# Optimization experiments

Hardware: AMD Instinct MI355X
Metric: run time of the kernel (lower is better)

## Reference

```python
import jax, jax.numpy as jnp
import numpy as np

B, V, H, K = 2048, 4096, 1024, 5

def setup_inputs() -> dict:
    key = jax.random.key(0)
    k1, k2, k3, k4, k5, k6, k7 = jax.random.split(key, 7)
    return {
        "visible_example": (jax.random.uniform(k1, (B, V)) > 0.5).astype(jnp.float32),
        "b_v": jax.random.normal(k2, (V,), jnp.float32) * 0.1,
        "b_h": jax.random.normal(k3, (H,), jnp.float32) * 0.1,
        "W": jax.random.normal(k4, (V, H), jnp.float32) * 0.02,
        "u_h0": jax.random.uniform(k5, (B, H), jnp.float32),
        "u_v": jax.random.uniform(k6, (K // 2 + 1, B, V), jnp.float32),
        "u_h": jax.random.uniform(k7, (K // 2, B, H), jnp.float32),
    }

def reference(visible_example, b_v, b_h, W, u_h0, u_v, u_h):
    # score(v,h) = -energy = v.b_v + h.b_h + (v @ W) * h summed
    def score(v, h):
        return v @ b_v + h @ b_h + jnp.einsum('bv,vh,bh->b', v, W, h)  # [B]

    def bernoulli(p, u):
        # samples are detached in the original (requires_grad_(False))
        return jax.lax.stop_gradient((p > u).astype(jnp.float32))

    # positive phase: sample h | data
    h = bernoulli(jax.nn.sigmoid(b_h + visible_example @ W), u_h0)  # [B,H]
    log_prob_positive = score(visible_example, h)

    # K-step alternating Gibbs chain: v, h, v, h, v  (statically unrolled)
    v = visible_example
    vi = hi = 0
    for k in range(K):
        if k % 2 == 0:
            v = bernoulli(jax.nn.sigmoid(b_v + h @ W.T), u_v[vi]); vi += 1
        else:
            h = bernoulli(jax.nn.sigmoid(b_h + v @ W), u_h[hi]); hi += 1

    log_prob_negative = score(v, h)
    return log_prob_positive - log_prob_negative  # [B]
```

## Files before the change

kernel.cpp:

```cpp
#include <hip/hip_runtime.h>
#include <math.h>

#define B_DIM 2048
#define V_DIM 4096
#define H_DIM 1024

#define BM 64
#define BN 64
#define BK 16
#define KC 384
#define LDS_STRIDE 68

enum { ACC_NONE = 0, ACC_PREACT = 1, ACC_BIAS = 2 };

__global__ __launch_bounds__(256) void gemm_h_kernel(
    const float* __restrict__ A,
    const float* __restrict__ W,
    const float* __restrict__ bh,
    const float* __restrict__ U,
    float* __restrict__ Hout,
    double* __restrict__ acc,
    const int mode)
{
    __shared__ float As[2][BK][LDS_STRIDE];
    __shared__ float Bs[2][BK][LDS_STRIDE];

    const int bn = blockIdx.x * BN;
    const int bm = blockIdx.y * BM;
    const int t  = threadIdx.x;
    const int tx = t & 15;
    const int ty = t >> 4;

    const int ar  = t >> 2;
    const int ac4 = t & 3;
    const int br  = t >> 4;
    const int bc4 = t & 15;

    float tot[4][4];
    float part[4][4];
#pragma unroll
    for (int i = 0; i < 4; i++)
#pragma unroll
        for (int j = 0; j < 4; j++) { tot[i][j] = 0.0f; part[i][j] = 0.0f; }

    const float* Aptr = A + (size_t)(bm + ar) * V_DIM + ac4 * 4;
    const float* Wptr = W + (size_t)bn + bc4 * 4;

    float4 av = *(const float4*)(Aptr + 0);
    float4 wv = *(const float4*)(Wptr + (size_t)br * H_DIM);
    As[0][ac4 * 4 + 0][ar] = av.x;
    As[0][ac4 * 4 + 1][ar] = av.y;
    As[0][ac4 * 4 + 2][ar] = av.z;
    As[0][ac4 * 4 + 3][ar] = av.w;
    *(float4*)(&Bs[0][br][bc4 * 4]) = wv;

    const int T = V_DIM / BK;
    int cur = 0;
    for (int it = 0; it < T; ++it) {
        __syncthreads();
        if (it + 1 < T) {
            const int k0 = (it + 1) * BK;
            av = *(const float4*)(Aptr + k0);
            wv = *(const float4*)(Wptr + (size_t)(k0 + br) * H_DIM);
        }
#pragma unroll
        for (int k = 0; k < BK; k++) {
            float4 a4 = *(const float4*)(&As[cur][k][ty * 4]);
            float4 b4 = *(const float4*)(&Bs[cur][k][tx * 4]);
            float aa[4] = {a4.x, a4.y, a4.z, a4.w};
            float bb[4] = {b4.x, b4.y, b4.z, b4.w};
#pragma unroll
            for (int i = 0; i < 4; i++)
#pragma unroll
                for (int j = 0; j < 4; j++)
                    part[i][j] = fmaf(aa[i], bb[j], part[i][j]);
        }
        if (it + 1 < T) {
            As[cur ^ 1][ac4 * 4 + 0][ar] = av.x;
            As[cur ^ 1][ac4 * 4 + 1][ar] = av.y;
            As[cur ^ 1][ac4 * 4 + 2][ar] = av.z;
            As[cur ^ 1][ac4 * 4 + 3][ar] = av.w;
            *(float4*)(&Bs[cur ^ 1][br][bc4 * 4]) = wv;
        }
        cur ^= 1;
        if ((((it + 1) * BK) % KC) == 0) {
#pragma unroll
            for (int i = 0; i < 4; i++)
#pragma unroll
                for (int j = 0; j < 4; j++) { tot[i][j] += part[i][j]; part[i][j] = 0.0f; }
        }
    }
    if ((V_DIM % KC) != 0) {
#pragma unroll
        for (int i = 0; i < 4; i++)
#pragma unroll
            for (int j = 0; j < 4; j++) tot[i][j] += part[i][j];
    }

    double rowacc[4] = {0.0, 0.0, 0.0, 0.0};
#pragma unroll
    for (int i = 0; i < 4; i++) {
        const int row = bm + ty * 4 + i;
#pragma unroll
        for (int j = 0; j < 4; j++) {
            const int col = bn + tx * 4 + j;
            float bias = bh[col];
            float pre = bias + tot[i][j];
            float p = 1.0f / (1.0f + expf(-pre));
            float u = U[(size_t)row * H_DIM + col];
            float hv = (p > u) ? 1.0f : 0.0f;
            Hout[(size_t)row * H_DIM + col] = hv;
            if (mode == ACC_PREACT) rowacc[i] += (double)hv * (double)pre;
            else if (mode == ACC_BIAS) rowacc[i] += (double)hv * (double)bias;
        }
    }
    if (mode != ACC_NONE) {
#pragma unroll
        for (int off = 8; off >= 1; off >>= 1)
#pragma unroll
            for (int i = 0; i < 4; i++)
                rowacc[i] += __shfl_xor(rowacc[i], off, 16);
        if (tx == 0) {
#pragma unroll
            for (int i = 0; i < 4; i++)
                atomicAdd(&acc[bm + ty * 4 + i], rowacc[i]);
        }
    }
}

__global__ __launch_bounds__(256) void gemm_v_kernel(
    const float* __restrict__ A,
    const float* __restrict__ W,
    const float* __restrict__ bv,
    const float* __restrict__ U,
    float* __restrict__ Vout,
    double* __restrict__ acc,
    const int mode)
{
    __shared__ float As[2][BK][LDS_STRIDE];
    __shared__ float Bs[2][BK][LDS_STRIDE];

    const int bn = blockIdx.x * BN;
    const int bm = blockIdx.y * BM;
    const int t  = threadIdx.x;
    const int tx = t & 15;
    const int ty = t >> 4;

    const int ar  = t >> 2;
    const int ac4 = t & 3;

    float tot[4][4];
    float part[4][4];
#pragma unroll
    for (int i = 0; i < 4; i++)
#pragma unroll
        for (int j = 0; j < 4; j++) { tot[i][j] = 0.0f; part[i][j] = 0.0f; }

    const float* Aptr = A + (size_t)(bm + ar) * H_DIM + ac4 * 4;
    const float* Wrow = W + (size_t)(bn + ar) * H_DIM + ac4 * 4;

    float4 av = *(const float4*)(Aptr + 0);
    float4 wv = *(const float4*)(Wrow + 0);
    As[0][ac4 * 4 + 0][ar] = av.x;
    As[0][ac4 * 4 + 1][ar] = av.y;
    As[0][ac4 * 4 + 2][ar] = av.z;
    As[0][ac4 * 4 + 3][ar] = av.w;
    Bs[0][ac4 * 4 + 0][ar] = wv.x;
    Bs[0][ac4 * 4 + 1][ar] = wv.y;
    Bs[0][ac4 * 4 + 2][ar] = wv.z;
    Bs[0][ac4 * 4 + 3][ar] = wv.w;

    const int T = H_DIM / BK;
    int cur = 0;
    for (int it = 0; it < T; ++it) {
        __syncthreads();
        if (it + 1 < T) {
            const int k0 = (it + 1) * BK;
            av = *(const float4*)(Aptr + k0);
            wv = *(const float4*)(Wrow + k0);
        }
#pragma unroll
        for (int k = 0; k < BK; k++) {
            float4 a4 = *(const float4*)(&As[cur][k][ty * 4]);
            float4 b4 = *(const float4*)(&Bs[cur][k][tx * 4]);
            float aa[4] = {a4.x, a4.y, a4.z, a4.w};
            float bb[4] = {b4.x, b4.y, b4.z, b4.w};
#pragma unroll
            for (int i = 0; i < 4; i++)
#pragma unroll
                for (int j = 0; j < 4; j++)
                    part[i][j] = fmaf(aa[i], bb[j], part[i][j]);
        }
        if (it + 1 < T) {
            As[cur ^ 1][ac4 * 4 + 0][ar] = av.x;
            As[cur ^ 1][ac4 * 4 + 1][ar] = av.y;
            As[cur ^ 1][ac4 * 4 + 2][ar] = av.z;
            As[cur ^ 1][ac4 * 4 + 3][ar] = av.w;
            Bs[cur ^ 1][ac4 * 4 + 0][ar] = wv.x;
            Bs[cur ^ 1][ac4 * 4 + 1][ar] = wv.y;
            Bs[cur ^ 1][ac4 * 4 + 2][ar] = wv.z;
            Bs[cur ^ 1][ac4 * 4 + 3][ar] = wv.w;
        }
        cur ^= 1;
        if ((((it + 1) * BK) % KC) == 0) {
#pragma unroll
            for (int i = 0; i < 4; i++)
#pragma unroll
                for (int j = 0; j < 4; j++) { tot[i][j] += part[i][j]; part[i][j] = 0.0f; }
        }
    }
    if ((H_DIM % KC) != 0) {
#pragma unroll
        for (int i = 0; i < 4; i++)
#pragma unroll
            for (int j = 0; j < 4; j++) tot[i][j] += part[i][j];
    }

    double rowacc[4] = {0.0, 0.0, 0.0, 0.0};
#pragma unroll
    for (int i = 0; i < 4; i++) {
        const int row = bm + ty * 4 + i;
#pragma unroll
        for (int j = 0; j < 4; j++) {
            const int col = bn + tx * 4 + j;
            float pre = bv[col] + tot[i][j];
            float p = 1.0f / (1.0f + expf(-pre));
            float u = U[(size_t)row * V_DIM + col];
            float vv = (p > u) ? 1.0f : 0.0f;
            Vout[(size_t)row * V_DIM + col] = vv;
            if (mode == ACC_PREACT) rowacc[i] += (double)vv * (double)pre;
        }
    }
    if (mode != ACC_NONE) {
#pragma unroll
        for (int off = 8; off >= 1; off >>= 1)
#pragma unroll
            for (int i = 0; i < 4; i++)
                rowacc[i] += __shfl_xor(rowacc[i], off, 16);
        if (tx == 0) {
#pragma unroll
            for (int i = 0; i < 4; i++)
                atomicAdd(&acc[bm + ty * 4 + i], rowacc[i]);
        }
    }
}

__global__ __launch_bounds__(256) void rowdot_kernel(
    const float* __restrict__ X, const float* __restrict__ w,
    double* __restrict__ out, const int N)
{
    const int b = blockIdx.x;
    const float* row = X + (size_t)b * N;
    double s = 0.0;
    for (int i = threadIdx.x; i < N / 4; i += blockDim.x) {
        float4 x = ((const float4*)row)[i];
        float4 ww = ((const float4*)w)[i];
        s = fma((double)x.x, (double)ww.x, s);
        s = fma((double)x.y, (double)ww.y, s);
        s = fma((double)x.z, (double)ww.z, s);
        s = fma((double)x.w, (double)ww.w, s);
    }
#pragma unroll
    for (int off = 32; off >= 1; off >>= 1) s += __shfl_xor(s, off, 64);
    __shared__ double red[4];
    if ((threadIdx.x & 63) == 0) red[threadIdx.x >> 6] = s;
    __syncthreads();
    if (threadIdx.x == 0) out[b] = red[0] + red[1] + red[2] + red[3];
}

__global__ void finalize_kernel(const double* __restrict__ vb,
                                const double* __restrict__ accpos,
                                const double* __restrict__ acchb,
                                const double* __restrict__ accneg,
                                float* __restrict__ out)
{
    int b = blockIdx.x * blockDim.x + threadIdx.x;
    if (b < B_DIM) out[b] = (float)(vb[b] + accpos[b] - acchb[b] - accneg[b]);
}

extern "C" void kernel_launch(void* const* d_in, const int* in_sizes, int n_in,
                              void* d_out, int out_size, void* d_ws, size_t ws_size,
                              hipStream_t stream) {
    (void)in_sizes; (void)n_in; (void)out_size; (void)ws_size;
    const float* visible = (const float*)d_in[0];
    const float* b_v     = (const float*)d_in[1];
    const float* b_h     = (const float*)d_in[2];
    const float* W       = (const float*)d_in[3];
    const float* u_h0    = (const float*)d_in[4];
    const float* u_v     = (const float*)d_in[5];
    const float* u_h     = (const float*)d_in[6];
    float* out = (float*)d_out;

    float* v_buf   = (float*)d_ws;
    float* h_buf   = v_buf + (size_t)B_DIM * V_DIM;
    double* acc_pos = (double*)(h_buf + (size_t)B_DIM * H_DIM);
    double* acc_hb  = acc_pos + B_DIM;
    double* acc_neg = acc_hb + B_DIM;
    double* vb      = acc_neg + B_DIM;

    hipMemsetAsync(acc_pos, 0, 3 * B_DIM * sizeof(double), stream);

    dim3 blk(256);
    dim3 gh(H_DIM / BN, B_DIM / BM);
    dim3 gv(V_DIM / BN, B_DIM / BM);

    rowdot_kernel<<<B_DIM, blk, 0, stream>>>(visible, b_v, vb, V_DIM);

    const size_t UV = (size_t)B_DIM * V_DIM;
    const size_t UH = (size_t)B_DIM * H_DIM;

    gemm_h_kernel<<<gh, blk, 0, stream>>>(visible, W, b_h, u_h0, h_buf, acc_pos, ACC_PREACT);
    gemm_v_kernel<<<gv, blk, 0, stream>>>(h_buf, W, b_v, u_v + 0 * UV, v_buf, nullptr, ACC_NONE);
    gemm_h_kernel<<<gh, blk, 0, stream>>>(v_buf, W, b_h, u_h + 0 * UH, h_buf, nullptr, ACC_NONE);
    gemm_v_kernel<<<gv, blk, 0, stream>>>(h_buf, W, b_v, u_v + 1 * UV, v_buf, nullptr, ACC_NONE);
    gemm_h_kernel<<<gh, blk, 0, stream>>>(v_buf, W, b_h, u_h + 1 * UH, h_buf, acc_hb, ACC_BIAS);
    gemm_v_kernel<<<gv, blk, 0, stream>>>(h_buf, W, b_v, u_v + 2 * UV, v_buf, acc_neg, ACC_PREACT);

    finalize_kernel<<<(B_DIM + 255) / 256, blk, 0, stream>>>(vb, acc_pos, acc_hb, acc_neg, out);
}
```

Measured before the change: 1.461 ms.

## Use 128x128 register tiles and split-K panels for the H-side GEMM

Raises the per-thread micro-tile from 4x4 to 8x8 (128x128 block tiles) in both GEMMs, so each LDS load feeds more FMAs. The B×V×H product for h has few blocks at this tile size, so it is split along K into 11 panels that write partial sums to a workspace. A separate combine kernel then reduces the panels, applies bias, sigmoid and sampling, and writes the row accumulators directly, replacing the atomics. This costs an extra write and read of 11 partial B×H buffers per h-step, plus higher register pressure from the 8x8 tiles.

```diff
diff --git a/kernel.cpp b/kernel.cpp
--- a/kernel.cpp
+++ b/kernel.cpp
@@ -5,126 +5,161 @@
 #define V_DIM 4096
 #define H_DIM 1024
 
-#define BM 64
-#define BN 64
+#define BM 128
+#define BN 128
 #define BK 16
 #define KC 384
-#define LDS_STRIDE 68
+#define NPANEL_H 11
+#define LDSS 132
 
 enum { ACC_NONE = 0, ACC_PREACT = 1, ACC_BIAS = 2 };
 
-__global__ __launch_bounds__(256) void gemm_h_kernel(
+__global__ __launch_bounds__(256) void gemm_h_panel(
     const float* __restrict__ A,
     const float* __restrict__ W,
+    float* __restrict__ P)
+{
+    __shared__ float As[2][BK][LDSS];
+    __shared__ float Bs[2][BK][LDSS];
+
+    const int bn  = blockIdx.x * BN;
+    const int bm  = blockIdx.y * BM;
+    const int pan = blockIdx.z;
+    const int k0  = pan * KC;
+    const int klen = (V_DIM - k0 < KC) ? (V_DIM - k0) : KC;
+    const int T = klen / BK;
+
+    const int t  = threadIdx.x;
+    const int tx = t & 15;
+    const int ty = t >> 4;
+
+    const int s_ar = t >> 1;
+    const int s_ak = (t & 1) * 8;
+    const int s_bc = (t & 31) * 4;
+    const int s_bk = t >> 5;
+
+    const float* Aptr = A + (size_t)(bm + s_ar) * V_DIM + k0 + s_ak;
+    const float* Wptr = W + (size_t)(k0 + s_bk) * H_DIM + bn + s_bc;
+
+    float part[8][8];
+#pragma unroll
+    for (int i = 0; i < 8; i++)
+#pragma unroll
+        for (int j = 0; j < 8; j++) part[i][j] = 0.0f;
+
+    float4 a0 = *(const float4*)(Aptr + 0);
+    float4 a1 = *(const float4*)(Aptr + 4);
+    float4 w0 = *(const float4*)(Wptr);
+    float4 w1 = *(const float4*)(Wptr + (size_t)8 * H_DIM);
+    As[0][s_ak + 0][s_ar] = a0.x;
+    As[0][s_ak + 1][s_ar] = a0.y;
+    As[0][s_ak + 2][s_ar] = a0.z;
+    As[0][s_ak + 3][s_ar] = a0.w;
+    As[0][s_ak + 4][s_ar] = a1.x;
+    As[0][s_ak + 5][s_ar] = a1.y;
+    As[0][s_ak + 6][s_ar] = a1.z;
+    As[0][s_ak + 7][s_ar] = a1.w;
+    *(float4*)(&Bs[0][s_bk][s_bc])     = w0;
+    *(float4*)(&Bs[0][s_bk + 8][s_bc]) = w1;
+
+    int cur = 0;
+    for (int it = 0; it < T; ++it) {
+        __syncthreads();
+        if (it + 1 < T) {
+            const int kk = (it + 1) * BK;
+            a0 = *(const float4*)(Aptr + kk);
+            a1 = *(const float4*)(Aptr + kk + 4);
+            w0 = *(const float4*)(Wptr + (size_t)kk * H_DIM);
+            w1 = *(const float4*)(Wptr + (size_t)(kk + 8) * H_DIM);
+        }
+#pragma unroll
+        for (int k = 0; k < BK; k++) {
+            float4 xa = *(const float4*)(&As[cur][k][ty * 4]);
+            float4 xb = *(const float4*)(&As[cur][k][64 + ty * 4]);
+            float4 ya = *(const float4*)(&Bs[cur][k][tx * 4]);
+            float4 yb = *(const float4*)(&Bs[cur][k][64 + tx * 4]);
+            float aa[8] = {xa.x, xa.y, xa.z, xa.w, xb.x, xb.y, xb.z, xb.w};
+            float bb[8] = {ya.x, ya.y, ya.z, ya.w, yb.x, yb.y, yb.z, yb.w};
+#pragma unroll
+            for (int i = 0; i < 8; i++)
+#pragma unroll
+                for (int j = 0; j < 8; j++)
+                    part[i][j] = fmaf(aa[i], bb[j], part[i][j]);
+        }
+        if (it + 1 < T) {
+            As[cur ^ 1][s_ak + 0][s_ar] = a0.x;
+            As[cur ^ 1][s_ak + 1][s_ar] = a0.y;
+            As[cur ^ 1][s_ak + 2][s_ar] = a0.z;
+            As[cur ^ 1][s_ak + 3][s_ar] = a0.w;
+            As[cur ^ 1][s_ak + 4][s_ar] = a1.x;
+            As[cur ^ 1][s_ak + 5][s_ar] = a1.y;
+            As[cur ^ 1][s_ak + 6][s_ar] = a1.z;
+            As[cur ^ 1][s_ak + 7][s_ar] = a1.w;
+            *(float4*)(&Bs[cur ^ 1][s_bk][s_bc])     = w0;
+            *(float4*)(&Bs[cur ^ 1][s_bk + 8][s_bc]) = w1;
+        }
+        cur ^= 1;
+    }
+
+    float* Pout = P + (size_t)pan * B_DIM * H_DIM;
+#pragma unroll
+    for (int i = 0; i < 8; i++) {
+        const int row = bm + ((i < 4) ? (ty * 4 + i) : (64 + ty * 4 + (i - 4)));
+        float4 lo, hi;
+        lo.x = part[i][0]; lo.y = part[i][1]; lo.z = part[i][2]; lo.w = part[i][3];
+        hi.x = part[i][4]; hi.y = part[i][5]; hi.z = part[i][6]; hi.w = part[i][7];
+        *(float4*)(&Pout[(size_t)row * H_DIM + bn + tx * 4])      = lo;
+        *(float4*)(&Pout[(size_t)row * H_DIM + bn + 64 + tx * 4]) = hi;
+    }
+}
+
+__global__ __launch_bounds__(256) void combine_h(
+    const float* __restrict__ P,
     const float* __restrict__ bh,
     const float* __restrict__ U,
     float* __restrict__ Hout,
     double* __restrict__ acc,
     const int mode)
 {
-    __shared__ float As[2][BK][LDS_STRIDE];
-    __shared__ float Bs[2][BK][LDS_STRIDE];
-
-    const int bn = blockIdx.x * BN;
-    const int bm = blockIdx.y * BM;
-    const int t  = threadIdx.x;
-    const int tx = t & 15;
-    const int ty = t >> 4;
-
-    const int ar  = t >> 2;
-    const int ac4 = t & 3;
-    const int br  = t >> 4;
-    const int bc4 = t & 15;
-
-    float tot[4][4];
-    float part[4][4];
-#pragma unroll
-    for (int i = 0; i < 4; i++)
-#pragma unroll
-        for (int j = 0; j < 4; j++) { tot[i][j] = 0.0f; part[i][j] = 0.0f; }
-
-    const float* Aptr = A + (size_t)(bm + ar) * V_DIM + ac4 * 4;
-    const float* Wptr = W + (size_t)bn + bc4 * 4;
-
-    float4 av = *(const float4*)(Aptr + 0);
-    float4 wv = *(const float4*)(Wptr + (size_t)br * H_DIM);
-    As[0][ac4 * 4 + 0][ar] = av.x;
-    As[0][ac4 * 4 + 1][ar] = av.y;
-    As[0][ac4 * 4 + 2][ar] = av.z;
-    As[0][ac4 * 4 + 3][ar] = av.w;
-    *(float4*)(&Bs[0][br][bc4 * 4]) = wv;
-
-    const int T = V_DIM / BK;
-    int cur = 0;
-    for (int it = 0; it < T; ++it) {
+    const int b = blockIdx.x;
+    const int c = threadIdx.x * 4;
+    const size_t BH  = (size_t)B_DIM * H_DIM;
+    const size_t off = (size_t)b * H_DIM + c;
+
+    float4 tot = *(const float4*)(P + off);
+#pragma unroll
+    for (int p = 1; p < NPANEL_H; p++) {
+        float4 q = *(const float4*)(P + (size_t)p * BH + off);
+        tot.x += q.x; tot.y += q.y; tot.z += q.z; tot.w += q.w;
+    }
+    float4 bias = *(const float4*)(bh + c);
+    float4 u    = *(const float4*)(U + off);
+
+    float pre[4] = {bias.x + tot.x, bias.y + tot.y, bias.z + tot.z, bias.w + tot.w};
+    float bb[4]  = {bias.x, bias.y, bias.z, bias.w};
+    float uu[4]  = {u.x, u.y, u.z, u.w};
+    float hv[4];
+#pragma unroll
+    for (int j = 0; j < 4; j++) {
+        float pp = 1.0f / (1.0f + expf(-pre[j]));
+        hv[j] = (pp > uu[j]) ? 1.0f : 0.0f;
+    }
+    float4 hout; hout.x = hv[0]; hout.y = hv[1]; hout.z = hv[2]; hout.w = hv[3];
+    *(float4*)(Hout + off) = hout;
+
+    if (mode != ACC_NONE) {
+        double s = 0.0;
+#pragma unroll
+        for (int j = 0; j < 4; j++) {
+            if (mode == ACC_PREACT) s += (double)hv[j] * (double)pre[j];
+            else                    s += (double)hv[j] * (double)bb[j];
+        }
+#pragma unroll
+        for (int offl = 32; offl >= 1; offl >>= 1) s += __shfl_xor(s, offl, 64);
+        __shared__ double red[4];
+        if ((threadIdx.x & 63) == 0) red[threadIdx.x >> 6] = s;
         __syncthreads();
-        if (it + 1 < T) {
-            const int k0 = (it + 1) * BK;
-            av = *(const float4*)(Aptr + k0);
-            wv = *(const float4*)(Wptr + (size_t)(k0 + br) * H_DIM);
-        }
-#pragma unroll
-        for (int k = 0; k < BK; k++) {
-            float4 a4 = *(const float4*)(&As[cur][k][ty * 4]);
-            float4 b4 = *(const float4*)(&Bs[cur][k][tx * 4]);
-            float aa[4] = {a4.x, a4.y, a4.z, a4.w};
-            float bb[4] = {b4.x, b4.y, b4.z, b4.w};
-#pragma unroll
-            for (int i = 0; i < 4; i++)
-#pragma unroll
-                for (int j = 0; j < 4; j++)
-                    part[i][j] = fmaf(aa[i], bb[j], part[i][j]);
-        }
-        if (it + 1 < T) {
-            As[cur ^ 1][ac4 * 4 + 0][ar] = av.x;
-            As[cur ^ 1][ac4 * 4 + 1][ar] = av.y;
-            As[cur ^ 1][ac4 * 4 + 2][ar] = av.z;
-            As[cur ^ 1][ac4 * 4 + 3][ar] = av.w;
-            *(float4*)(&Bs[cur ^ 1][br][bc4 * 4]) = wv;
-        }
-        cur ^= 1;
-        if ((((it + 1) * BK) % KC) == 0) {
-#pragma unroll
-            for (int i = 0; i < 4; i++)
-#pragma unroll
-                for (int j = 0; j < 4; j++) { tot[i][j] += part[i][j]; part[i][j] = 0.0f; }
-        }
-    }
-    if ((V_DIM % KC) != 0) {
-#pragma unroll
-        for (int i = 0; i < 4; i++)
-#pragma unroll
-            for (int j = 0; j < 4; j++) tot[i][j] += part[i][j];
-    }
-
-    double rowacc[4] = {0.0, 0.0, 0.0, 0.0};
-#pragma unroll
-    for (int i = 0; i < 4; i++) {
-        const int row = bm + ty * 4 + i;
-#pragma unroll
-        for (int j = 0; j < 4; j++) {
-            const int col = bn + tx * 4 + j;
-            float bias = bh[col];
-            float pre = bias + tot[i][j];
-            float p = 1.0f / (1.0f + expf(-pre));
-            float u = U[(size_t)row * H_DIM + col];
-            float hv = (p > u) ? 1.0f : 0.0f;
-            Hout[(size_t)row * H_DIM + col] = hv;
-            if (mode == ACC_PREACT) rowacc[i] += (double)hv * (double)pre;
-            else if (mode == ACC_BIAS) rowacc[i] += (double)hv * (double)bias;
-        }
-    }
-    if (mode != ACC_NONE) {
-#pragma unroll
-        for (int off = 8; off >= 1; off >>= 1)
-#pragma unroll
-            for (int i = 0; i < 4; i++)
-                rowacc[i] += __shfl_xor(rowacc[i], off, 16);
-        if (tx == 0) {
-#pragma unroll
-            for (int i = 0; i < 4; i++)
-                atomicAdd(&acc[bm + ty * 4 + i], rowacc[i]);
-        }
+        if (threadIdx.x == 0) acc[b] = red[0] + red[1] + red[2] + red[3];
     }
 }
 
@@ -137,8 +172,8 @@
     double* __restrict__ acc,
     const int mode)
 {
-    __shared__ float As[2][BK][LDS_STRIDE];
-    __shared__ float Bs[2][BK][LDS_STRIDE];
+    __shared__ float As[2][BK][LDSS];
+    __shared__ float Bs[2][BK][LDSS];
 
     const int bn = blockIdx.x * BN;
     const int bm = blockIdx.y * BM;
@@ -146,101 +181,133 @@
     const int tx = t & 15;
     const int ty = t >> 4;
 
-    const int ar  = t >> 2;
-    const int ac4 = t & 3;
-
-    float tot[4][4];
-    float part[4][4];
-#pragma unroll
-    for (int i = 0; i < 4; i++)
-#pragma unroll
-        for (int j = 0; j < 4; j++) { tot[i][j] = 0.0f; part[i][j] = 0.0f; }
-
-    const float* Aptr = A + (size_t)(bm + ar) * H_DIM + ac4 * 4;
-    const float* Wrow = W + (size_t)(bn + ar) * H_DIM + ac4 * 4;
-
-    float4 av = *(const float4*)(Aptr + 0);
-    float4 wv = *(const float4*)(Wrow + 0);
-    As[0][ac4 * 4 + 0][ar] = av.x;
-    As[0][ac4 * 4 + 1][ar] = av.y;
-    As[0][ac4 * 4 + 2][ar] = av.z;
-    As[0][ac4 * 4 + 3][ar] = av.w;
-    Bs[0][ac4 * 4 + 0][ar] = wv.x;
-    Bs[0][ac4 * 4 + 1][ar] = wv.y;
-    Bs[0][ac4 * 4 + 2][ar] = wv.z;
-    Bs[0][ac4 * 4 + 3][ar] = wv.w;
+    const int s_ar = t >> 1;
+    const int s_ak = (t & 1) * 8;
+
+    const float* Aptr = A + (size_t)(bm + s_ar) * H_DIM + s_ak;
+    const float* Wrow = W + (size_t)(bn + s_ar) * H_DIM + s_ak;
+
+    float tot[8][8];
+    float part[8][8];
+#pragma unroll
+    for (int i = 0; i < 8; i++)
+#pragma unroll
+        for (int j = 0; j < 8; j++) { tot[i][j] = 0.0f; part[i][j] = 0.0f; }
+
+    float4 a0 = *(const float4*)(Aptr + 0);
+    float4 a1 = *(const float4*)(Aptr + 4);
+    float4 w0 = *(const float4*)(Wrow + 0);
+    float4 w1 = *(const float4*)(Wrow + 4);
+    As[0][s_ak + 0][s_ar] = a0.x;
+    As[0][s_ak + 1][s_ar] = a0.y;
+    As[0][s_ak + 2][s_ar] = a0.z;
+    As[0][s_ak + 3][s_ar] = a0.w;
+    As[0][s_ak + 4][s_ar] = a1.x;
+    As[0][s_ak + 5][s_ar] = a1.y;
+    As[0][s_ak + 6][s_ar] = a1.z;
+    As[0][s_ak + 7][s_ar] = a1.w;
+    Bs[0][s_ak + 0][s_ar] = w0.x;
+    Bs[0][s_ak + 1][s_ar] = w0.y;
+    Bs[0][s_ak + 2][s_ar] = w0.z;
+    Bs[0][s_ak + 3][s_ar] = w0.w;
+    Bs[0][s_ak + 4][s_ar] = w1.x;
+    Bs[0][s_ak + 5][s_ar] = w1.y;
+    Bs[0][s_ak + 6][s_ar] = w1.z;
+    Bs[0][s_ak + 7][s_ar] = w1.w;
 
     const int T = H_DIM / BK;
     int cur = 0;
     for (int it = 0; it < T; ++it) {
         __syncthreads();
         if (it + 1 < T) {
-            const int k0 = (it + 1) * BK;
-            av = *(const float4*)(Aptr + k0);
-            wv = *(const float4*)(Wrow + k0);
+            const int kk = (it + 1) * BK;
+            a0 = *(const float4*)(Aptr + kk);
+            a1 = *(const float4*)(Aptr + kk + 4);
+            w0 = *(const float4*)(Wrow + kk);
+            w1 = *(const float4*)(Wrow + kk + 4);
         }
 #pragma unroll
         for (int k = 0; k < BK; k++) {
-            float4 a4 = *(const float4*)(&As[cur][k][ty * 4]);
-            float4 b4 = *(const float4*)(&Bs[cur][k][tx * 4]);
-            float aa[4] = {a4.x, a4.y, a4.z, a4.w};
-            float bb[4] = {b4.x, b4.y, b4.z, b4.w};
-#pragma unroll
-            for (int i = 0; i < 4; i++)
-#pragma unroll
-                for (int j = 0; j < 4; j++)
+            float4 xa = *(const float4*)(&As[cur][k][ty * 4]);
+            float4 xb = *(const float4*)(&As[cur][k][64 + ty * 4]);
+            float4 ya = *(const float4*)(&Bs[cur][k][tx * 4]);
+            float4 yb = *(const float4*)(&Bs[cur][k][64 + tx * 4]);
+            float aa[8] = {xa.x, xa.y, xa.z, xa.w, xb.x, xb.y, xb.z, xb.w};
+            float bb[8] = {ya.x, ya.y, ya.z, ya.w, yb.x, yb.y, yb.z, yb.w};
+#pragma unroll
+            for (int i = 0; i < 8; i++)
+#pragma unroll
+                for (int j = 0; j < 8; j++)
                     part[i][j] = fmaf(aa[i], bb[j], part[i][j]);
         }
         if (it + 1 < T) {
-            As[cur ^ 1][ac4 * 4 + 0][ar] = av.x;
-            As[cur ^ 1][ac4 * 4 + 1][ar] = av.y;
-            As[cur ^ 1][ac4 * 4 + 2][ar] = av.z;
-            As[cur ^ 1][ac4 * 4 + 3][ar] = av.w;
-            Bs[cur ^ 1][ac4 * 4 + 0][ar] = wv.x;
-            Bs[cur ^ 1][ac4 * 4 + 1][ar] = wv.y;
-            Bs[cur ^ 1][ac4 * 4 + 2][ar] = wv.z;
-            Bs[cur ^ 1][ac4 * 4 + 3][ar] = wv.w;
+            As[cur ^ 1][s_ak + 0][s_ar] = a0.x;
+            As[cur ^ 1][s_ak + 1][s_ar] = a0.y;
+            As[cur ^ 1][s_ak + 2][s_ar] = a0.z;
+            As[cur ^ 1][s_ak + 3][s_ar] = a0.w;
+            As[cur ^ 1][s_ak + 4][s_ar] = a1.x;
+            As[cur ^ 1][s_ak + 5][s_ar] = a1.y;
+            As[cur ^ 1][s_ak + 6][s_ar] = a1.z;
+            As[cur ^ 1][s_ak + 7][s_ar] = a1.w;
+            Bs[cur ^ 1][s_ak + 0][s_ar] = w0.x;
+            Bs[cur ^ 1][s_ak + 1][s_ar] = w0.y;
+            Bs[cur ^ 1][s_ak + 2][s_ar] = w0.z;
+            Bs[cur ^ 1][s_ak + 3][s_ar] = w0.w;
+            Bs[cur ^ 1][s_ak + 4][s_ar] = w1.x;
+            Bs[cur ^ 1][s_ak + 5][s_ar] = w1.y;
+            Bs[cur ^ 1][s_ak + 6][s_ar] = w1.z;
+            Bs[cur ^ 1][s_ak + 7][s_ar] = w1.w;
         }
         cur ^= 1;
         if ((((it + 1) * BK) % KC) == 0) {
 #pragma unroll
-            for (int i = 0; i < 4; i++)
-#pragma unroll
-                for (int j = 0; j < 4; j++) { tot[i][j] += part[i][j]; part[i][j] = 0.0f; }
+            for (int i = 0; i < 8; i++)
+#pragma unroll
+                for (int j = 0; j < 8; j++) { tot[i][j] += part[i][j]; part[i][j] = 0.0f; }
         }
     }
     if ((H_DIM % KC) != 0) {
 #pragma unroll
-        for (int i = 0; i < 4; i++)
-#pragma unroll
-            for (int j = 0; j < 4; j++) tot[i][j] += part[i][j];
-    }
-
-    double rowacc[4] = {0.0, 0.0, 0.0, 0.0};
-#pragma unroll
-    for (int i = 0; i < 4; i++) {
-        const int row = bm + ty * 4 + i;
-#pragma unroll
-        for (int j = 0; j < 4; j++) {
-            const int col = bn + tx * 4 + j;
-            float pre = bv[col] + tot[i][j];
-            float p = 1.0f / (1.0f + expf(-pre));
-            float u = U[(size_t)row * V_DIM + col];
-            float vv = (p > u) ? 1.0f : 0.0f;
-            Vout[(size_t)row * V_DIM + col] = vv;
-            if (mode == ACC_PREACT) rowacc[i] += (double)vv * (double)pre;
+        for (int i = 0; i < 8; i++)
+#pragma unroll
+            for (int j = 0; j < 8; j++) tot[i][j] += part[i][j];
+    }
+
+    double rowacc[8] = {0, 0, 0, 0, 0, 0, 0, 0};
+#pragma unroll
+    for (int i = 0; i < 8; i++) {
+        const int row = bm + ((i < 4) ? (ty * 4 + i) : (64 + ty * 4 + (i - 4)));
+#pragma unroll
+        for (int jj = 0; jj < 2; jj++) {
+            const int col0 = bn + ((jj == 0) ? (tx * 4) : (64 + tx * 4));
+            float4 u4 = *(const float4*)(&U[(size_t)row * V_DIM + col0]);
+            float uu[4] = {u4.x, u4.y, u4.z, u4.w};
+            float4 vstore;
+            float vs[4];
+#pragma unroll
+            for (int j = 0; j < 4; j++) {
+                float pre = bv[col0 + j] + tot[i][jj * 4 + j];
+                float p = 1.0f / (1.0f + expf(-pre));
+                float vv = (p > uu[j]) ? 1.0f : 0.0f;
+                vs[j] = vv;
+                if (mode == ACC_PREACT) rowacc[i] += (double)vv * (double)pre;
+            }
+            vstore.x = vs[0]; vstore.y = vs[1]; vstore.z = vs[2]; vstore.w = vs[3];
+            *(float4*)(&Vout[(size_t)row * V_DIM + col0]) = vstore;
         }
     }
     if (mode != ACC_NONE) {
 #pragma unroll
         for (int off = 8; off >= 1; off >>= 1)
 #pragma unroll
-            for (int i = 0; i < 4; i++)
+            for (int i = 0; i < 8; i++)
                 rowacc[i] += __shfl_xor(rowacc[i], off, 16);
         if (tx == 0) {
 #pragma unroll
-            for (int i = 0; i < 4; i++)
-                atomicAdd(&acc[bm + ty * 4 + i], rowacc[i]);
+            for (int i = 0; i < 8; i++) {
+                const int row = bm + ((i < 4) ? (ty * 4 + i) : (64 + ty * 4 + (i - 4)));
+                atomicAdd(&acc[row], rowacc[i]);
+            }
         }
     }
 }
@@ -297,23 +364,28 @@
     double* acc_hb  = acc_pos + B_DIM;
     double* acc_neg = acc_hb + B_DIM;
     double* vb      = acc_neg + B_DIM;
-
-    hipMemsetAsync(acc_pos, 0, 3 * B_DIM * sizeof(double), stream);
+    float* Ppart    = (float*)(vb + B_DIM);
+
+    hipMemsetAsync(acc_neg, 0, B_DIM * sizeof(double), stream);
 
     dim3 blk(256);
-    dim3 gh(H_DIM / BN, B_DIM / BM);
+    dim3 gh(H_DIM / BN, B_DIM / BM, NPANEL_H);
     dim3 gv(V_DIM / BN, B_DIM / BM);
+    dim3 gc(B_DIM);
 
     rowdot_kernel<<<B_DIM, blk, 0, stream>>>(visible, b_v, vb, V_DIM);
 
     const size_t UV = (size_t)B_DIM * V_DIM;
     const size_t UH = (size_t)B_DIM * H_DIM;
 
-    gemm_h_kernel<<<gh, blk, 0, stream>>>(visible, W, b_h, u_h0, h_buf, acc_pos, ACC_PREACT);
+    gemm_h_panel<<<gh, blk, 0, stream>>>(visible, W, Ppart);
+    combine_h<<<gc, blk, 0, stream>>>(Ppart, b_h, u_h0, h_buf, acc_pos, ACC_PREACT);
     gemm_v_kernel<<<gv, blk, 0, stream>>>(h_buf, W, b_v, u_v + 0 * UV, v_buf, nullptr, ACC_NONE);
-    gemm_h_kernel<<<gh, blk, 0, stream>>>(v_buf, W, b_h, u_h + 0 * UH, h_buf, nullptr, ACC_NONE);
+    gemm_h_panel<<<gh, blk, 0, stream>>>(v_buf, W, Ppart);
+    combine_h<<<gc, blk, 0, stream>>>(Ppart, b_h, u_h + 0 * UH, h_buf, nullptr, ACC_NONE);
     gemm_v_kernel<<<gv, blk, 0, stream>>>(h_buf, W, b_v, u_v + 1 * UV, v_buf, nullptr, ACC_NONE);
-    gemm_h_kernel<<<gh, blk, 0, stream>>>(v_buf, W, b_h, u_h + 1 * UH, h_buf, acc_hb, ACC_BIAS);
+    gemm_h_panel<<<gh, blk, 0, stream>>>(v_buf, W, Ppart);
+    combine_h<<<gc, blk, 0, stream>>>(Ppart, b_h, u_h + 1 * UH, h_buf, acc_hb, ACC_BIAS);
     gemm_v_kernel<<<gv, blk, 0, stream>>>(h_buf, W, b_v, u_v + 2 * UV, v_buf, acc_neg, ACC_PREACT);
 
     finalize_kernel<<<(B_DIM + 255) / 256, blk, 0, stream>>>(vb, acc_pos, acc_hb, acc_neg, out);
```

After: 1.856 ms. +27.0%, slower.
